# Kernel tuning notes

Measured on AMD Instinct MI355X. Metric: run time of the kernel, lower is better.

Reference implementation:

```python
import jax, jax.numpy as jnp
import numpy as np

HIDDEN = 5120
HEAD_DIM = 128
HQ = 40
HKV = 8
NUM_MOD = 3
Q_SIZE = HQ * HEAD_DIM          # 5120
KV_SIZE = HKV * HEAD_DIM        # 1024
GATE = HQ                       # attn gating enabled
QKV_OUT = Q_SIZE + 2 * KV_SIZE + GATE  # 7208
EPS = 1e-6
N_TOK = 2048


def setup_inputs() -> dict:
    key = jax.random.key(0)
    ks = jax.random.split(key, 8)
    s = 0.02
    return {
        "hidden_states": jax.random.normal(ks[0], (N_TOK, HIDDEN), jnp.float32),
        "rope": jax.random.normal(ks[1], (N_TOK, HEAD_DIM), jnp.float32),
        "pre_norm_w": jax.random.normal(ks[2], (NUM_MOD * HIDDEN,), jnp.float32) * s,
        "qkv_w": jax.random.normal(ks[3], (NUM_MOD * QKV_OUT, HIDDEN), jnp.float32) * s,
        "q_norm_w": jax.random.normal(ks[4], (NUM_MOD * HEAD_DIM,), jnp.float32) * s,
        "k_norm_w": jax.random.normal(ks[5], (NUM_MOD * HEAD_DIM,), jnp.float32) * s,
        "proj_w": jax.random.normal(ks[6], (NUM_MOD * HIDDEN, Q_SIZE), jnp.float32) * s,
        "modality_ids": jax.random.randint(ks[7], (N_TOK,), 0, NUM_MOD, jnp.int64),
    }


def _mm_rmsnorm(x, w_flat, mids, dim):
    # per-token modality weight slice; residual parameterization (w + 1)
    w = w_flat.reshape(NUM_MOD, dim)[mids]  # [N, dim]
    if x.ndim == 3:
        w = w[:, None, :]  # broadcast over heads
    rms = jax.lax.rsqrt(jnp.mean(x * x, axis=-1, keepdims=True) + EPS)
    return x * rms * (w + 1.0)


def _moe_linear(x, w_flat, mids, out_f):
    # 3 GEMMs (one per expert), then per-token select -- same math as masked dispatch
    wm = w_flat.reshape(NUM_MOD, out_f, x.shape[-1])
    outs = jnp.einsum('nd,mod->nmo', x, wm)  # [N, 3, out_f]
    return jnp.take_along_axis(outs, mids[:, None, None], axis=1)[:, 0, :]


def _rotary(x, cos, sin):
    # x: [N, H, D]; cos/sin: [N, D/2]
    x1, x2 = jnp.split(x, 2, axis=-1)
    c = cos[:, None, :]
    s = sin[:, None, :]
    return jnp.concatenate([x1 * c - x2 * s, x1 * s + x2 * c], axis=-1)


def reference(hidden_states, rope, pre_norm_w, qkv_w, q_norm_w, k_norm_w, proj_w, modality_ids):
    N = hidden_states.shape[0]
    mids = modality_ids

    h = _mm_rmsnorm(hidden_states, pre_norm_w, mids, HIDDEN)
    qkv = _moe_linear(h, qkv_w, mids, QKV_OUT)  # [N, 7208]
    q, k, v, g = jnp.split(qkv, [Q_SIZE, Q_SIZE + KV_SIZE, Q_SIZE + 2 * KV_SIZE], axis=-1)
    q = q.reshape(N, HQ, HEAD_DIM)
    k = k.reshape(N, HKV, HEAD_DIM)
    v = v.reshape(N, HKV, HEAD_DIM)

    q = _mm_rmsnorm(q, q_norm_w, mids, HEAD_DIM)
    k = _mm_rmsnorm(k, k_norm_w, mids, HEAD_DIM)

    sin, cos = jnp.split(rope, 2, axis=-1)  # rope.chunk(2, dim=-1) -> sin, cos
    q = _rotary(q, cos, sin)
    k = _rotary(k, cos, sin)

    # GQA attention over the full token sequence
    G = HQ // HKV
    qg = q.reshape(N, HKV, G, HEAD_DIM)
    scale = 1.0 / np.sqrt(HEAD_DIM).astype(np.float32)
    scores = jnp.einsum('nkgd,mkd->kgnm', qg, k) * scale  # [8, 5, N, N]
    p = jax.nn.softmax(scores, axis=-1)
    o = jnp.einsum('kgnm,mkd->nkgd', p, v).reshape(N, HQ, HEAD_DIM)

    o = o * jax.nn.sigmoid(g)[:, :, None]  # attention gating per q-head
    o = o.reshape(N, Q_SIZE)
    return _moe_linear(o, proj_w, mids, HIDDEN)
```

## Files before the change

kernel.cpp:

```cpp
#include <hip/hip_runtime.h>
#include <hip/hip_bf16.h>

#define N_TOK 2048
#define HIDDEN 5120
#define HEAD_DIM 128
#define HQ 40
#define HKV 8
#define QKV_OUT 7208
#define Q_SIZE 5120
#define KV_SIZE 1024

typedef __attribute__((ext_vector_type(8))) short bf16x8;
typedef __attribute__((ext_vector_type(4))) float f32x4;
typedef __attribute__((ext_vector_type(4))) unsigned short us4;

__device__ inline unsigned short f2bf(float f) {
    return __builtin_bit_cast(unsigned short, __float2bfloat16(f));
}
__device__ inline float bf2f(unsigned short s) {
    unsigned u = ((unsigned)s) << 16;
    return __builtin_bit_cast(float, u);
}
__device__ inline f32x4 mfma16(bf16x8 a, bf16x8 b, f32x4 c) {
    return __builtin_amdgcn_mfma_f32_16x16x32_bf16(a, b, c, 0, 0, 0);
}
__device__ inline void gl16(const void* g, void* l) {
    __builtin_amdgcn_global_load_lds((__attribute__((address_space(1))) void*)g,
                                     (__attribute__((address_space(3))) void*)l, 16, 0, 0);
}

__global__ void k_sort(const int* __restrict__ mids_raw, int* __restrict__ meta,
                       int* __restrict__ perm) {
    int l = threadIdx.x;
    int oddnz = 0;
    for (int c = 0; c < 32; ++c) {
        int idx = c * 64 + l;
        int v = mids_raw[idx];
        if ((idx & 1) && v != 0) oddnz = 1;
    }
    bool is64 = (__ballot(oddnz) == 0ULL);
    int c0 = 0, c1 = 0;
    for (int c = 0; c < 32; ++c) {
        int i = c * 64 + l;
        int m = is64 ? mids_raw[2 * i] : mids_raw[i];
        c0 += (m == 0); c1 += (m == 1);
    }
    for (int o = 32; o; o >>= 1) { c0 += __shfl_xor(c0, o); c1 += __shfl_xor(c1, o); }
    if (l == 0) { meta[0] = 0; meta[1] = c0; meta[2] = c0 + c1; meta[3] = N_TOK; }
    int r0 = 0, r1 = c0, r2 = c0 + c1;
    unsigned long long below = (1ULL << l) - 1ULL;
    for (int c = 0; c < 32; ++c) {
        int i = c * 64 + l;
        int m = is64 ? mids_raw[2 * i] : mids_raw[i];
        unsigned long long b0 = __ballot(m == 0), b1 = __ballot(m == 1), b2 = __ballot(m == 2);
        int pos = (m == 0) ? r0 + __popcll(b0 & below)
                : (m == 1) ? r1 + __popcll(b1 & below)
                           : r2 + __popcll(b2 & below);
        perm[pos] = i;
        r0 += __popcll(b0); r1 += __popcll(b1); r2 += __popcll(b2);
    }
}

__global__ __launch_bounds__(256) void k_cvt(const float* __restrict__ src,
                                             unsigned short* __restrict__ dst, int n8) {
    int i = blockIdx.x * 256 + threadIdx.x;
    int stride = gridDim.x * 256;
    for (; i < n8; i += stride) {
        float4 a = ((const float4*)src)[2 * i];
        float4 b = ((const float4*)src)[2 * i + 1];
        bf16x8 o;
        o[0] = (short)f2bf(a.x); o[1] = (short)f2bf(a.y);
        o[2] = (short)f2bf(a.z); o[3] = (short)f2bf(a.w);
        o[4] = (short)f2bf(b.x); o[5] = (short)f2bf(b.y);
        o[6] = (short)f2bf(b.z); o[7] = (short)f2bf(b.w);
        ((bf16x8*)dst)[i] = o;
    }
}

__global__ __launch_bounds__(256) void k_prenorm(const float* __restrict__ hidden,
        const float* __restrict__ pnw, const int* __restrict__ meta,
        const int* __restrict__ perm, unsigned short* __restrict__ h) {
    int i = blockIdx.x;
    int m = (i >= meta[1]) + (i >= meta[2]);
    int t = perm[i];
    const float4* x = (const float4*)(hidden + (size_t)t * HIDDEN);
    const float4* wv = (const float4*)(pnw + (size_t)m * HIDDEN);
    int tid = threadIdx.x;
    float4 xv[5];
    float ss = 0.f;
#pragma unroll
    for (int j = 0; j < 5; ++j) {
        xv[j] = x[tid + j * 256];
        ss += xv[j].x * xv[j].x + xv[j].y * xv[j].y + xv[j].z * xv[j].z + xv[j].w * xv[j].w;
    }
    for (int o = 32; o; o >>= 1) ss += __shfl_xor(ss, o);
    __shared__ float red[4];
    if ((tid & 63) == 0) red[tid >> 6] = ss;
    __syncthreads();
    float rms = rsqrtf((red[0] + red[1] + red[2] + red[3]) * (1.f / HIDDEN) + 1e-6f);
    us4* dst = (us4*)(h + (size_t)i * HIDDEN);
#pragma unroll
    for (int j = 0; j < 5; ++j) {
        float4 w = wv[tid + j * 256];
        us4 o4;
        o4.x = f2bf(xv[j].x * rms * (w.x + 1.f));
        o4.y = f2bf(xv[j].y * rms * (w.y + 1.f));
        o4.z = f2bf(xv[j].z * rms * (w.z + 1.f));
        o4.w = f2bf(xv[j].w * rms * (w.w + 1.f));
        dst[tid + j * 256] = o4;
    }
}

template <int NOUT, bool SCATTER>
__global__ __launch_bounds__(256) void k_gemm(
        const unsigned short* __restrict__ A, const unsigned short* __restrict__ Bw,
        unsigned short* __restrict__ outB, float* __restrict__ outF,
        const int* __restrict__ meta, const int* __restrict__ perm,
        int nx, int ny) {
    int nwg = nx * ny * 3;
    int bid = blockIdx.x;
    int xcd = bid & 7, o = bid >> 3;
    int q = nwg >> 3, r = nwg & 7;
    int swz = (xcd < r ? xcd * (q + 1) : r * (q + 1) + (xcd - r) * q) + o;
    int mz = swz / (nx * ny);
    int rest = swz - mz * (nx * ny);
    int ty = rest / nx, tx = rest - ty * nx;

    int rowS = meta[mz], rowE = meta[mz + 1];
    int row0 = rowS + tx * 128;
    if (row0 >= rowE) return;
    int col0 = ty * 128;
    const unsigned short* Bm = Bw + (size_t)mz * NOUT * HIDDEN;

    __shared__ __align__(16) unsigned short As[128 * 64];
    __shared__ __align__(16) unsigned short Bs[128 * 64];
    int tid = threadIdx.x, l = tid & 63, w = tid >> 6;
    int wr = (w >> 1) * 64, wc = (w & 1) * 64;

    f32x4 acc[4][4] = {};

    const int lr = l >> 3, lc = l & 7;
    const int sch = (lc ^ lr) * 8;
    const unsigned short* ag[4];
    const unsigned short* bg[4];
#pragma unroll
    for (int j = 0; j < 4; ++j) {
        int ar = row0 + 32 * j + 8 * w + lr;
        if (ar > rowE - 1) ar = rowE - 1;
        ag[j] = A + (size_t)ar * HIDDEN + sch;
        int bc = col0 + 32 * j + 8 * w + lr;
        if (bc > NOUT - 1) bc = NOUT - 1;
        bg[j] = Bm + (size_t)bc * HIDDEN + sch;
    }
    char* asw = (char*)As + w * 1024;
    char* bsw = (char*)Bs + w * 1024;

#pragma unroll 1
    for (int kk = 0; kk < HIDDEN; kk += 64) {
#pragma unroll
        for (int j = 0; j < 4; ++j) {
            gl16(ag[j] + kk, asw + j * 4096);
            gl16(bg[j] + kk, bsw + j * 4096);
        }
        __syncthreads();
#pragma unroll
        for (int ks = 0; ks < 2; ++ks) {
            bf16x8 af[4], bfm[4];
#pragma unroll
            for (int mi = 0; mi < 4; ++mi) {
                int row = wr + mi * 16 + (l & 15);
                af[mi] = *(const bf16x8*)((char*)As + row * 128 +
                            ((ks * 64 + (l >> 4) * 16) ^ ((row & 7) << 4)));
            }
#pragma unroll
            for (int ni = 0; ni < 4; ++ni) {
                int row = wc + ni * 16 + (l & 15);
                bfm[ni] = *(const bf16x8*)((char*)Bs + row * 128 +
                            ((ks * 64 + (l >> 4) * 16) ^ ((row & 7) << 4)));
            }
#pragma unroll
            for (int mi = 0; mi < 4; ++mi)
#pragma unroll
                for (int ni = 0; ni < 4; ++ni)
                    acc[mi][ni] = mfma16(af[mi], bfm[ni], acc[mi][ni]);
        }
        __syncthreads();
    }
#pragma unroll
    for (int mi = 0; mi < 4; ++mi) {
        int rbase = row0 + wr + mi * 16 + ((l >> 4) << 2);
#pragma unroll
        for (int ni = 0; ni < 4; ++ni) {
            int col = col0 + wc + ni * 16 + (l & 15);
            if (col >= NOUT) continue;
#pragma unroll
            for (int rr = 0; rr < 4; ++rr) {
                int row = rbase + rr;
                if (row >= rowE) continue;
                if (SCATTER) {
                    int t = perm[row];
                    outF[(size_t)t * HIDDEN + col] = acc[mi][ni][rr];
                } else {
                    outB[(size_t)row * NOUT + col] = f2bf(acc[mi][ni][rr]);
                }
            }
        }
    }
}

template <int NOUT, bool SCATTER>
__global__ __launch_bounds__(256) void k_moe_gemm(
        const unsigned short* __restrict__ A, const float* __restrict__ B,
        unsigned short* __restrict__ outB, float* __restrict__ outF,
        const int* __restrict__ meta, const int* __restrict__ perm) {
    int mz = blockIdx.z;
    int rowS = meta[mz], rowE = meta[mz + 1];
    int row0 = rowS + blockIdx.y * 128;
    if (row0 >= rowE) return;
    int col0 = blockIdx.x * 128;
    const float* Bm = B + (size_t)mz * NOUT * HIDDEN;

    __shared__ __align__(16) unsigned short As[128 * 64];
    __shared__ __align__(16) unsigned short Bs[128 * 64];
    int tid = threadIdx.x, l = tid & 63, w = tid >> 6;
    int wr = (w >> 1) * 64, wc = (w & 1) * 64;

    f32x4 acc[4][4] = {};
    int sr = tid >> 1, half = tid & 1;
    int arow = row0 + sr;
    if (arow > N_TOK - 1) arow = N_TOK - 1;
    const unsigned short* aptr = A + (size_t)arow * HIDDEN + half * 32;
    int bcol = col0 + sr;
    bool bok = (bcol < NOUT);
    const float* bptr = Bm + (size_t)(bok ? bcol : 0) * HIDDEN + half * 32;

    char* awp[4]; char* bwp[4];
#pragma unroll
    for (int q = 0; q < 4; ++q) {
        int boff = sr * 128 + ((((half * 4 + q) * 16)) ^ ((sr & 7) << 4));
        awp[q] = (char*)As + boff;
        bwp[q] = (char*)Bs + boff;
    }

#pragma unroll 1
    for (int kk = 0; kk < HIDDEN; kk += 64) {
        bf16x8 av[4];
#pragma unroll
        for (int q = 0; q < 4; ++q) av[q] = *(const bf16x8*)(aptr + kk + q * 8);
        bf16x8 bw[4];
#pragma unroll
        for (int q = 0; q < 4; ++q) {
            float4 u, v;
            if (bok) {
                u = ((const float4*)(bptr + kk))[2 * q];
                v = ((const float4*)(bptr + kk))[2 * q + 1];
            } else {
                u = make_float4(0.f, 0.f, 0.f, 0.f);
                v = u;
            }
            bf16x8 pk;
            pk[0] = (short)f2bf(u.x); pk[1] = (short)f2bf(u.y);
            pk[2] = (short)f2bf(u.z); pk[3] = (short)f2bf(u.w);
            pk[4] = (short)f2bf(v.x); pk[5] = (short)f2bf(v.y);
            pk[6] = (short)f2bf(v.z); pk[7] = (short)f2bf(v.w);
            bw[q] = pk;
        }
        __syncthreads();
#pragma unroll
        for (int q = 0; q < 4; ++q) {
            *(bf16x8*)awp[q] = av[q];
            *(bf16x8*)bwp[q] = bw[q];
        }
        __syncthreads();
#pragma unroll
        for (int ks = 0; ks < 2; ++ks) {
            bf16x8 af[4], bfm[4];
#pragma unroll
            for (int mi = 0; mi < 4; ++mi) {
                int row = wr + mi * 16 + (l & 15);
                af[mi] = *(const bf16x8*)((char*)As + row * 128 +
                            ((ks * 64 + (l >> 4) * 16) ^ ((row & 7) << 4)));
            }
#pragma unroll
            for (int ni = 0; ni < 4; ++ni) {
                int row = wc + ni * 16 + (l & 15);
                bfm[ni] = *(const bf16x8*)((char*)Bs + row * 128 +
                            ((ks * 64 + (l >> 4) * 16) ^ ((row & 7) << 4)));
            }
#pragma unroll
            for (int mi = 0; mi < 4; ++mi)
#pragma unroll
                for (int ni = 0; ni < 4; ++ni)
                    acc[mi][ni] = mfma16(af[mi], bfm[ni], acc[mi][ni]);
        }
    }
#pragma unroll
    for (int mi = 0; mi < 4; ++mi) {
        int rbase = row0 + wr + mi * 16 + ((l >> 4) << 2);
#pragma unroll
        for (int ni = 0; ni < 4; ++ni) {
            int col = col0 + wc + ni * 16 + (l & 15);
            if (col >= NOUT) continue;
#pragma unroll
            for (int rr = 0; rr < 4; ++rr) {
                int row = rbase + rr;
                if (row >= rowE) continue;
                if (SCATTER) {
                    int t = perm[row];
                    outF[(size_t)t * HIDDEN + col] = acc[mi][ni][rr];
                } else {
                    outB[(size_t)row * NOUT + col] = f2bf(acc[mi][ni][rr]);
                }
            }
        }
    }
}

__global__ __launch_bounds__(256) void k_qknorm(const unsigned short* __restrict__ qkv,
        const float* __restrict__ rope, const float* __restrict__ qnw,
        const float* __restrict__ knw, const int* __restrict__ meta,
        const int* __restrict__ perm, unsigned short* __restrict__ qb,
        unsigned short* __restrict__ kb, float* __restrict__ gate) {
    int i = blockIdx.x;
    int m = (i >= meta[1]) + (i >= meta[2]);
    int t = perm[i];
    int tid = threadIdx.x, w = tid >> 6, l = tid & 63;
    const unsigned short* base = qkv + (size_t)i * QKV_OUT;
    const float* rp = rope + (size_t)t * HEAD_DIM;
    const float qscale = 0.08838834764831845f * 1.4426950408889634f;
    for (int hh = w; hh < 48; hh += 4) {
        bool isq = hh < 40;
        const unsigned short* src = base + (isq ? hh * 128 : Q_SIZE + (hh - 40) * 128);
        float x0 = bf2f(src[2 * l]), x1 = bf2f(src[2 * l + 1]);
        float ss = x0 * x0 + x1 * x1;
        for (int o = 32; o; o >>= 1) ss += __shfl_xor(ss, o);
        float rms = rsqrtf(ss * (1.f / 128.f) + 1e-6f);
        const float* nw = (isq ? qnw : knw) + m * 128;
        float y0 = x0 * rms * (nw[2 * l] + 1.f);
        float y1 = x1 * rms * (nw[2 * l + 1] + 1.f);
        float p0 = __shfl_xor(y0, 32);
        float p1 = __shfl_xor(y1, 32);
        float r0v, r1v;
        if (l < 32) {
            int d = 2 * l;
            r0v = y0 * rp[64 + d] - p0 * rp[d];
            r1v = y1 * rp[64 + d + 1] - p1 * rp[d + 1];
        } else {
            int d = 2 * l - 64;
            r0v = p0 * rp[d] + y0 * rp[64 + d];
            r1v = p1 * rp[d + 1] + y1 * rp[64 + d + 1];
        }
        if (isq) {
            r0v *= qscale; r1v *= qscale;
            unsigned short* dst = qb + (size_t)i * Q_SIZE + hh * 128 + 2 * l;
            dst[0] = f2bf(r0v); dst[1] = f2bf(r1v);
        } else {
            unsigned short* dst = kb + (size_t)i * KV_SIZE + (hh - 40) * 128 + 2 * l;
            dst[0] = f2bf(r0v); dst[1] = f2bf(r1v);
        }
    }
    if (tid < HQ) {
        float g = bf2f(base[Q_SIZE + 2 * KV_SIZE + tid]);
        gate[(size_t)i * HQ + tid] = 1.f / (1.f + expf(-g));
    }
}

__global__ __launch_bounds__(256) void k_vtrans(const unsigned short* __restrict__ qkv,
                                                unsigned short* __restrict__ vT) {
    int t0 = blockIdx.x * 64, db = blockIdx.y * 64, kvh = blockIdx.z;
    __shared__ unsigned short tile[64][68];
    int tid = threadIdx.x;
    int tr = tid >> 2, seg = tid & 3;
    const unsigned short* src = qkv + (size_t)(t0 + tr) * QKV_OUT + Q_SIZE + KV_SIZE +
                                kvh * 128 + db + seg * 16;
    us4* drow = (us4*)&tile[tr][seg * 16];
#pragma unroll
    for (int q = 0; q < 4; ++q) drow[q] = ((const us4*)src)[q];
    __syncthreads();
    int dr = tid >> 2;
    unsigned short* dst = vT + ((size_t)kvh * 128 + db + dr) * N_TOK + t0 + seg * 16;
    unsigned short buf[16];
#pragma unroll
    for (int j = 0; j < 16; ++j) buf[j] = tile[seg * 16 + j][dr];
#pragma unroll
    for (int q = 0; q < 4; ++q) ((us4*)dst)[q] = ((us4*)buf)[q];
}

__global__ __launch_bounds__(256) void k_attn(
        const unsigned short* __restrict__ qb,
        const unsigned short* __restrict__ kb,
        const unsigned short* __restrict__ vT,
        const float* __restrict__ gate,
        unsigned short* __restrict__ og) {
    int qt = blockIdx.x, qh = blockIdx.y, kvh = qh / 5;
    int tid = threadIdx.x, w = tid >> 6, l = tid & 63;
    int q0 = qt * 128 + w * 32;
    __shared__ __align__(16) char smem[49152];
    char* Ks = smem;
    char* Vs = smem + 16384;
    char* Ps = smem + 32768 + w * 4096;

    bf16x8 qf[2][4];
#pragma unroll
    for (int mi = 0; mi < 2; ++mi)
#pragma unroll
        for (int ks = 0; ks < 4; ++ks)
            qf[mi][ks] = *(const bf16x8*)(qb + (size_t)(q0 + mi * 16 + (l & 15)) * Q_SIZE +
                                          qh * 128 + ks * 32 + (l >> 4) * 8);

    f32x4 oacc[2][8] = {};
    f32x4 psum[2] = {};

    int kr = tid >> 2, kseg = tid & 3;
    int vr = tid >> 1, vh2 = tid & 1;

#pragma unroll 1
    for (int kt = 0; kt < 32; ++kt) {
        int t0 = kt * 64;
        bf16x8 kv4[4], vv4[4];
        const unsigned short* ksrc = kb + (size_t)(t0 + kr) * KV_SIZE + kvh * 128 + kseg * 32;
        const unsigned short* vsrc = vT + ((size_t)kvh * 128 + vr) * N_TOK + t0 + vh2 * 32;
#pragma unroll
        for (int q = 0; q < 4; ++q) {
            kv4[q] = *(const bf16x8*)(ksrc + q * 8);
            vv4[q] = *(const bf16x8*)(vsrc + q * 8);
        }
        __syncthreads();
#pragma unroll
        for (int q = 0; q < 4; ++q) {
            *(bf16x8*)(Ks + kr * 256 + ((((kseg * 4 + q) * 16)) ^ ((kr & 7) << 4))) = kv4[q];
            *(bf16x8*)(Vs + vr * 128 + ((((vh2 * 4 + q) * 16)) ^ ((vr & 7) << 4))) = vv4[q];
        }
        __syncthreads();
        f32x4 s[2][4] = {};
#pragma unroll
        for (int ks = 0; ks < 4; ++ks) {
            bf16x8 kf[4];
#pragma unroll
            for (int ni = 0; ni < 4; ++ni) {
                int row = ni * 16 + (l & 15);
                kf[ni] = *(const bf16x8*)(Ks + row * 256 +
                            ((ks * 64 + (l >> 4) * 16) ^ ((row & 7) << 4)));
            }
#pragma unroll
            for (int mi = 0; mi < 2; ++mi)
#pragma unroll
                for (int ni = 0; ni < 4; ++ni)
                    s[mi][ni] = mfma16(qf[mi][ks], kf[ni], s[mi][ni]);
        }
#pragma unroll
        for (int mi = 0; mi < 2; ++mi)
#pragma unroll
            for (int ni = 0; ni < 4; ++ni) {
#pragma unroll
                for (int r = 0; r < 4; ++r) {
                    float p = exp2f(s[mi][ni][r]);
                    psum[mi][r] += p;
                    int qr = mi * 16 + ((l >> 4) << 2) + r;
                    int tcb = (ni * 16 + (l & 15)) * 2;
                    *(unsigned short*)(Ps + qr * 128 +
                        (tcb ^ (((qr >> 2) & 3) << 5))) = f2bf(p);
                }
            }
#pragma unroll
        for (int ks = 0; ks < 2; ++ks) {
            bf16x8 pa[2];
#pragma unroll
            for (int mi = 0; mi < 2; ++mi) {
                int qr = mi * 16 + (l & 15);
                pa[mi] = *(const bf16x8*)(Ps + qr * 128 +
                            ((ks * 64 + (l >> 4) * 16) ^ (((qr >> 2) & 3) << 5)));
            }
#pragma unroll
            for (int nd = 0; nd < 8; ++nd) {
                int row = nd * 16 + (l & 15);
                bf16x8 vf = *(const bf16x8*)(Vs + row * 128 +
                            ((ks * 64 + (l >> 4) * 16) ^ ((row & 7) << 4)));
#pragma unroll
                for (int mi = 0; mi < 2; ++mi)
                    oacc[mi][nd] = mfma16(pa[mi], vf, oacc[mi][nd]);
            }
        }
    }
#pragma unroll
    for (int mi = 0; mi < 2; ++mi)
#pragma unroll
        for (int r = 0; r < 4; ++r) {
            float v = psum[mi][r];
            v += __shfl_xor(v, 1);
            v += __shfl_xor(v, 2);
            v += __shfl_xor(v, 4);
            v += __shfl_xor(v, 8);
            psum[mi][r] = v;
        }
#pragma unroll
    for (int mi = 0; mi < 2; ++mi)
#pragma unroll
        for (int r = 0; r < 4; ++r) {
            int row = q0 + mi * 16 + ((l >> 4) << 2) + r;
            float sc = (1.f / psum[mi][r]) * gate[(size_t)row * HQ + qh];
#pragma unroll
            for (int nd = 0; nd < 8; ++nd)
                og[(size_t)row * Q_SIZE + qh * 128 + nd * 16 + (l & 15)] =
                    f2bf(oacc[mi][nd][r] * sc);
        }
}

extern "C" void kernel_launch(void* const* d_in, const int* in_sizes, int n_in,
                              void* d_out, int out_size, void* d_ws, size_t ws_size,
                              hipStream_t stream) {
    const float* hidden = (const float*)d_in[0];
    const float* rope   = (const float*)d_in[1];
    const float* pnw    = (const float*)d_in[2];
    const float* qkvw   = (const float*)d_in[3];
    const float* qnw    = (const float*)d_in[4];
    const float* knw    = (const float*)d_in[5];
    const float* projw  = (const float*)d_in[6];
    const int*   mids   = (const int*)d_in[7];
    float* out = (float*)d_out;

    char* ws = (char*)d_ws;
    const size_t nqkvw = (size_t)3 * QKV_OUT * HIDDEN;
    const size_t nprojw = (size_t)3 * HIDDEN * Q_SIZE;
    const size_t wbytes = (nqkvw + nprojw) * 2;

    const size_t small_bytes = 16384 +
        (size_t)N_TOK * HIDDEN * 2 +
        (size_t)N_TOK * QKV_OUT * 2 +
        (size_t)N_TOK * Q_SIZE * 2 +
        (size_t)N_TOK * KV_SIZE * 2 +
        (size_t)N_TOK * KV_SIZE * 2 +
        (size_t)N_TOK * Q_SIZE * 2 +
        (size_t)N_TOK * HQ * 4;
    bool use_bf = (ws_size >= wbytes + small_bytes);
    if (!use_bf && ws_size < small_bytes) return;

    unsigned short* wqkv = (unsigned short*)ws;
    unsigned short* wproj = wqkv + nqkvw;
    char* sb = ws + (use_bf ? wbytes : 0);

    int* meta = (int*)sb;
    int* perm = (int*)(sb + 64);
    unsigned short* h   = (unsigned short*)(sb + 16384);
    unsigned short* qkv = h   + (size_t)N_TOK * HIDDEN;
    unsigned short* qb  = qkv + (size_t)N_TOK * QKV_OUT;
    unsigned short* kb  = qb  + (size_t)N_TOK * Q_SIZE;
    unsigned short* vT  = kb  + (size_t)N_TOK * KV_SIZE;
    unsigned short* og  = vT  + (size_t)N_TOK * KV_SIZE;
    float* gate = (float*)(og + (size_t)N_TOK * Q_SIZE);

    k_sort<<<1, 64, 0, stream>>>(mids, meta, perm);
    if (use_bf) {
        k_cvt<<<2048, 256, 0, stream>>>(qkvw, wqkv, (int)(nqkvw / 8));
        k_cvt<<<2048, 256, 0, stream>>>(projw, wproj, (int)(nprojw / 8));
    }
    k_prenorm<<<2048, 256, 0, stream>>>(hidden, pnw, meta, perm, h);
    if (use_bf)
        k_gemm<QKV_OUT, false><<<16 * 57 * 3, 256, 0, stream>>>(
            h, wqkv, qkv, nullptr, meta, perm, 16, 57);
    else
        k_moe_gemm<QKV_OUT, false><<<dim3(57, 16, 3), 256, 0, stream>>>(
            h, qkvw, qkv, nullptr, meta, perm);
    k_qknorm<<<2048, 256, 0, stream>>>(qkv, rope, qnw, knw, meta, perm, qb, kb, gate);
    k_vtrans<<<dim3(32, 2, 8), 256, 0, stream>>>(qkv, vT);
    k_attn<<<dim3(16, 40), 256, 0, stream>>>(qb, kb, vT, gate, og);
    if (use_bf)
        k_gemm<HIDDEN, true><<<16 * 40 * 3, 256, 0, stream>>>(
            og, wproj, nullptr, out, meta, perm, 16, 40);
    else
        k_moe_gemm<HIDDEN, true><<<dim3(40, 16, 3), 256, 0, stream>>>(
            og, projw, nullptr, out, meta, perm);
}
```

Baseline: 1.076 ms.

## Double-buffer LDS tiles in MoE GEMM to overlap global loads with MFMA

The GEMM main loop now uses two LDS buffers. The next K-tile's direct global-to-LDS loads are issued before computing on the current tile, and there is one barrier per iteration instead of two. The goal is to hide global memory latency behind MFMA work. LDS use grows to 64 KB per block, which limits how many blocks fit per CU, and launch bounds now ask for 2 waves-per-EU occupancy.

```diff
diff --git a/kernel.cpp b/kernel.cpp
--- a/kernel.cpp
+++ b/kernel.cpp
@@ -112,7 +112,7 @@
 }
 
 template <int NOUT, bool SCATTER>
-__global__ __launch_bounds__(256) void k_gemm(
+__global__ __launch_bounds__(256, 2) void k_gemm(
         const unsigned short* __restrict__ A, const unsigned short* __restrict__ Bw,
         unsigned short* __restrict__ outB, float* __restrict__ outF,
         const int* __restrict__ meta, const int* __restrict__ perm,
@@ -132,8 +132,7 @@
     int col0 = ty * 128;
     const unsigned short* Bm = Bw + (size_t)mz * NOUT * HIDDEN;
 
-    __shared__ __align__(16) unsigned short As[128 * 64];
-    __shared__ __align__(16) unsigned short Bs[128 * 64];
+    __shared__ __align__(16) char smem[65536];
     int tid = threadIdx.x, l = tid & 63, w = tid >> 6;
     int wr = (w >> 1) * 64, wc = (w & 1) * 64;
 
@@ -152,30 +151,32 @@
         if (bc > NOUT - 1) bc = NOUT - 1;
         bg[j] = Bm + (size_t)bc * HIDDEN + sch;
     }
-    char* asw = (char*)As + w * 1024;
-    char* bsw = (char*)Bs + w * 1024;
-
-#pragma unroll 1
-    for (int kk = 0; kk < HIDDEN; kk += 64) {
+    char* asw = smem + w * 1024;
+    char* bsw = smem + 16384 + w * 1024;
+
+    auto STAGE = [&](int buf, int kk) {
 #pragma unroll
         for (int j = 0; j < 4; ++j) {
-            gl16(ag[j] + kk, asw + j * 4096);
-            gl16(bg[j] + kk, bsw + j * 4096);
-        }
-        __syncthreads();
+            gl16(ag[j] + kk, asw + buf * 32768 + j * 4096);
+            gl16(bg[j] + kk, bsw + buf * 32768 + j * 4096);
+        }
+    };
+    auto COMPUTE = [&](int buf) {
+        char* baseA = smem + buf * 32768;
+        char* baseB = baseA + 16384;
 #pragma unroll
         for (int ks = 0; ks < 2; ++ks) {
             bf16x8 af[4], bfm[4];
 #pragma unroll
             for (int mi = 0; mi < 4; ++mi) {
                 int row = wr + mi * 16 + (l & 15);
-                af[mi] = *(const bf16x8*)((char*)As + row * 128 +
+                af[mi] = *(const bf16x8*)(baseA + row * 128 +
                             ((ks * 64 + (l >> 4) * 16) ^ ((row & 7) << 4)));
             }
 #pragma unroll
             for (int ni = 0; ni < 4; ++ni) {
                 int row = wc + ni * 16 + (l & 15);
-                bfm[ni] = *(const bf16x8*)((char*)Bs + row * 128 +
+                bfm[ni] = *(const bf16x8*)(baseB + row * 128 +
                             ((ks * 64 + (l >> 4) * 16) ^ ((row & 7) << 4)));
             }
 #pragma unroll
@@ -184,8 +185,26 @@
                 for (int ni = 0; ni < 4; ++ni)
                     acc[mi][ni] = mfma16(af[mi], bfm[ni], acc[mi][ni]);
         }
-        __syncthreads();
-    }
+    };
+
+    STAGE(0, 0);
+    asm volatile("s_waitcnt vmcnt(0)" ::: "memory");
+    __builtin_amdgcn_sched_barrier(0);
+    __builtin_amdgcn_s_barrier();
+    __builtin_amdgcn_sched_barrier(0);
+    int cur = 0;
+#pragma unroll 1
+    for (int kt = 0; kt < HIDDEN / 64 - 1; ++kt) {
+        STAGE(cur ^ 1, (kt + 1) * 64);
+        COMPUTE(cur);
+        asm volatile("s_waitcnt vmcnt(0) lgkmcnt(0)" ::: "memory");
+        __builtin_amdgcn_sched_barrier(0);
+        __builtin_amdgcn_s_barrier();
+        __builtin_amdgcn_sched_barrier(0);
+        cur ^= 1;
+    }
+    COMPUTE(cur);
+
 #pragma unroll
     for (int mi = 0; mi < 4; ++mi) {
         int rbase = row0 + wr + mi * 16 + ((l >> 4) << 2);
```

Result: faster. 958.6 us (-10.9%).
